# Optimization experiments

Hardware: AMD Instinct MI355X
Metric: run time of the kernel (lower is better)

## Reference

```python
import jax, jax.numpy as jnp
import numpy as np

C = 256       # in_channels
INTER = C // 2
BS = 4        # block_size
BN_EPS = 1e-5


def _conv1x1(x, w, b):
    # x: [N,C,H,W], w: [O,C], b: [O]
    return jnp.einsum('nchw,oc->nohw', x, w) + b[None, :, None, None]


def _maxpool2(x):
    n, c, h, w = x.shape
    return x.reshape(n, c, h // 2, 2, w // 2, 2).max(axis=(3, 5))


def setup_inputs() -> dict:
    key = jax.random.key(0)
    ks = jax.random.split(key, 13)
    p = lambda k, shape, s=0.05: jax.random.normal(k, shape, jnp.float32) * s
    return {
        'x': jax.random.normal(ks[0], (8, C, 128, 128), jnp.float32),
        'theta_w': p(ks[1], (INTER, C)), 'theta_b': p(ks[2], (INTER,)),
        'phi_w': p(ks[3], (INTER, C)), 'phi_b': p(ks[4], (INTER,)),
        'g_w': p(ks[5], (INTER, C)), 'g_b': p(ks[6], (INTER,)),
        'w_w': p(ks[7], (C, INTER)), 'w_b': p(ks[8], (C,)),
        'bn_gamma': p(ks[9], (C,)), 'bn_beta': p(ks[10], (C,)),
        'bn_mean': p(ks[11], (C,)), 'bn_var': jnp.abs(p(ks[12], (C,))) + 1.0,
    }


def reference(x, theta_w, theta_b, phi_w, phi_b, g_w, g_b, w_w, w_b,
              bn_gamma, bn_beta, bn_mean, bn_var):
    b, c, h, w = x.shape
    th, tw = h // BS, w // BS  # tile size (32,32)
    # split into BS*BS non-overlapping tiles, batch them: [b*BS*BS, c, th, tw]
    xb = x.reshape(b, c, BS, th, BS, tw).transpose(0, 2, 4, 1, 3, 5)
    xb = xb.reshape(b * BS * BS, c, th, tw)
    # SNLB (batched over all tiles at once)
    theta = _conv1x1(xb, theta_w, theta_b).reshape(-1, INTER, th * tw).transpose(0, 2, 1)  # [N,q,i]
    phi = _maxpool2(_conv1x1(xb, phi_w, phi_b)).reshape(-1, INTER, (th // 2) * (tw // 2))   # [N,i,k]
    g = _maxpool2(_conv1x1(xb, g_w, g_b)).reshape(-1, INTER, (th // 2) * (tw // 2))
    g = g.transpose(0, 2, 1)                                                                # [N,k,i]
    f = jax.nn.softmax(jnp.einsum('nqi,nik->nqk', theta, phi), axis=-1)                     # [N,q,k]
    y = jnp.einsum('nqk,nki->nqi', f, g).transpose(0, 2, 1).reshape(-1, INTER, th, tw)
    wy = _conv1x1(y, w_w, w_b)
    inv = jax.lax.rsqrt(bn_var + BN_EPS)
    wy = (wy - bn_mean[None, :, None, None]) * (inv * bn_gamma)[None, :, None, None] \
         + bn_beta[None, :, None, None]
    z = wy + xb  # [N,c,th,tw]
    # torch: cat tiles along channel dim (tile-major), then view(b, c, th*BS, -1)
    bf = z.reshape(b, BS * BS * c, th, tw)
    return bf.reshape(b, c, th * BS, -1)
```

## Files before the change

### kernel.cpp

```cpp
#include <hip/hip_runtime.h>
#include <hip/hip_bf16.h>

typedef __bf16 bf16_t;
typedef __bf16 bf16x8 __attribute__((ext_vector_type(8)));
typedef float f32x4 __attribute__((ext_vector_type(4)));

#define LDT 136
#define LDF 264
#define LDP 136
#define LDG 264

__device__ __forceinline__ float ldin(const void* p, long i, int isbf) {
  if (isbf) {
    unsigned short u = ((const unsigned short*)p)[i];
    unsigned int w = ((unsigned int)u) << 16;
    float f; __builtin_memcpy(&f, &w, 4); return f;
  }
  return ((const float*)p)[i];
}

__device__ __forceinline__ bf16_t f2b(float f) {
  unsigned int u; __builtin_memcpy(&u, &f, 4);
  u += 0x7FFFu + ((u >> 16) & 1u);
  unsigned short h = (unsigned short)(u >> 16);
  bf16_t r; __builtin_memcpy(&r, &h, 2); return r;
}

__device__ __forceinline__ float b2f(bf16_t b) {
  unsigned short h; __builtin_memcpy(&h, &b, 2);
  unsigned int u = ((unsigned int)h) << 16;
  float f; __builtin_memcpy(&f, &u, 4); return f;
}

__device__ __forceinline__ float bb2f(unsigned short h) {
  unsigned int u = ((unsigned int)h) << 16;
  float f; __builtin_memcpy(&f, &u, 4); return f;
}

__device__ __forceinline__ unsigned short bbits(bf16_t b) {
  unsigned short h; __builtin_memcpy(&h, &b, 2); return h;
}

__device__ __forceinline__ void ld4(const void* p, long i, int isbf, float* v) {
  if (isbf) {
    ushort4 u = *(const ushort4*)((const unsigned short*)p + i);
    v[0] = bb2f(u.x); v[1] = bb2f(u.y); v[2] = bb2f(u.z); v[3] = bb2f(u.w);
  } else {
    float4 f = *(const float4*)((const float*)p + i);
    v[0] = f.x; v[1] = f.y; v[2] = f.z; v[3] = f.w;
  }
}

__device__ __forceinline__ f32x4 mfma(bf16x8 a, bf16x8 b, f32x4 c) {
  return __builtin_amdgcn_mfma_f32_16x16x32_bf16(a, b, c, 0, 0, 0);
}

__global__ void kdetect(const unsigned int* x, int* flag) {
  __shared__ int cnt;
  if (threadIdx.x == 0) cnt = 0;
  __syncthreads();
  int local = 0;
  for (int k = 0; k < 4; ++k) {
    unsigned int u = x[threadIdx.x * 4 + k];
    unsigned int e = (u >> 7) & 0xFFu;
    if (e >= 116u && e <= 133u) local++;
  }
  atomicAdd(&cnt, local);
  __syncthreads();
  if (threadIdx.x == 0) *flag = (cnt > 512) ? 1 : 0;
}

__global__ void k0(const void* thw_f, const void* phw, const void* gw, const void* ww_f,
                   const void* wb, const void* gma, const void* bta, const void* mean,
                   const void* var, bf16_t* thwb, bf16_t* phwb, bf16_t* gwb, bf16_t* wwb,
                   float* scw, float* shw, const int* flag) {
  int isbf = *flag;
  int i = blockIdx.x * 256 + threadIdx.x;
  thwb[i] = f2b(ldin(thw_f, i, isbf));
  phwb[i] = f2b(ldin(phw, i, isbf));
  gwb[i]  = f2b(ldin(gw, i, isbf));
  wwb[i]  = f2b(ldin(ww_f, i, isbf));
  if (i < 256) {
    float s = ldin(gma, i, isbf) * rsqrtf(ldin(var, i, isbf) + 1e-5f);
    scw[i] = s;
    shw[i] = (ldin(wb, i, isbf) - ldin(mean, i, isbf)) * s + ldin(bta, i, isbf);
  }
}

__global__ __launch_bounds__(256) void k1(const void* xin, const bf16_t* phwb,
    const bf16_t* gwb, const void* phb, const void* gbb,
    bf16_t* phiH, bf16_t* phiL, bf16_t* gT, const int* flag) {
  int isbf = *flag;
  int wg = blockIdx.x;
  int tile = wg >> 4, j = wg & 15;
  int bi = tile >> 4, t16 = tile & 15, ty = t16 >> 2, tx = t16 & 3;
  long xb = (long)bi * 256 * 16384 + (long)(ty * 32 + 2 * j) * 128 + tx * 32;

  __shared__ __align__(16) bf16_t sX[64 * 256];
  __shared__ __align__(16) bf16_t sPoH[16 * 136];
  __shared__ __align__(16) bf16_t sPoL[16 * 136];
  __shared__ __align__(16) bf16_t sGo[128 * 24];

  int tid = threadIdx.x, lane = tid & 63, wv = tid >> 6;
  int qd = lane >> 4, ln = lane & 15, kq = qd * 8;

  bf16x8 Bp[8], Bg[8];
  {
    const bf16_t* bp = phwb + (wv * 16 + ln) * 256;
    const bf16_t* bg = gwb + (wv * 16 + ln) * 256;
    #pragma unroll
    for (int c = 0; c < 8; ++c) {
      Bp[c] = *(const bf16x8*)(bp + c * 32 + kq);
      Bg[c] = *(const bf16x8*)(bg + c * 32 + kq);
    }
  }

  {
    int mq = tid & 15, c0 = tid >> 4;
    int ma = (mq >> 3) * 128 + (mq & 7) * 4;
    #pragma unroll
    for (int it = 0; it < 16; ++it) {
      int c = it * 16 + c0;
      float v[4];
      ld4(xin, xb + (long)c * 16384 + ma, isbf, v);
      #pragma unroll
      for (int r = 0; r < 4; ++r) {
        int m = mq * 4 + r;
        int s = (((m >> 2) ^ m) & 7) << 3;
        sX[m * 256 + (c ^ s)] = f2b(v[r]);
      }
    }
  }
  __syncthreads();

  #pragma unroll
  for (int h = 0; h < 2; ++h) {
    if (h == 1) {
      const bf16_t* bp = phwb + ((wv + 4) * 16 + ln) * 256;
      const bf16_t* bg = gwb + ((wv + 4) * 16 + ln) * 256;
      #pragma unroll
      for (int c = 0; c < 8; ++c) {
        Bp[c] = *(const bf16x8*)(bp + c * 32 + kq);
        Bg[c] = *(const bf16x8*)(bg + c * 32 + kq);
      }
    }
    f32x4 accP[4], accG[4];
    #pragma unroll
    for (int mb = 0; mb < 4; ++mb) {
      int row = mb * 16 + ln;
      int s = (((row >> 2) ^ row) & 7) << 3;
      bf16x8 af[8];
      #pragma unroll
      for (int c = 0; c < 8; ++c)
        af[c] = *(const bf16x8*)(sX + row * 256 + ((c * 32 + kq) ^ s));
      f32x4 ap = {0.f,0.f,0.f,0.f}, ag = {0.f,0.f,0.f,0.f};
      #pragma unroll
      for (int c = 0; c < 8; ++c) {
        ap = mfma(af[c], Bp[c], ap);
        ag = mfma(af[c], Bg[c], ag);
      }
      accP[mb] = ap; accG[mb] = ag;
    }
    int o = (wv + h * 4) * 16 + ln;
    float pb = ldin(phb, o, isbf), gb2 = ldin(gbb, o, isbf);
    #pragma unroll
    for (int mb2 = 0; mb2 < 2; ++mb2)
      #pragma unroll
      for (int r = 0; r < 4; r += 2) {
        float v = fmaxf(fmaxf(accP[mb2][r], accP[mb2][r + 1]),
                        fmaxf(accP[mb2 + 2][r], accP[mb2 + 2][r + 1]));
        float u = fmaxf(fmaxf(accG[mb2][r], accG[mb2][r + 1]),
                        fmaxf(accG[mb2 + 2][r], accG[mb2 + 2][r + 1]));
        int cp = mb2 * 8 + qd * 2 + (r >> 1);
        float pv = v + pb;
        bf16_t hi = f2b(pv);
        sPoH[cp * 136 + o] = hi;
        sPoL[cp * 136 + o] = f2b(pv - b2f(hi));
        sGo[o * 24 + cp] = f2b(u + gb2);
      }
  }
  __syncthreads();

  {
    int kp = tid >> 4, seg = tid & 15;
    long base = (long)tile * 32768 + (long)(j * 16 + kp) * 128 + seg * 8;
    *(uint4*)(phiH + base) = *(const uint4*)(sPoH + kp * 136 + seg * 8);
    *(uint4*)(phiL + base) = *(const uint4*)(sPoL + kp * 136 + seg * 8);
  }
  {
    int o = tid >> 1, sg = tid & 1;
    *(uint4*)(gT + (long)tile * 32768 + (long)o * 256 + j * 16 + sg * 8) =
        *(const uint4*)(sGo + o * 24 + sg * 8);
  }
}

__global__ __launch_bounds__(256, 3) void k2(const void* xin, const bf16_t* thwb,
    const void* thb, const bf16_t* phiH, const bf16_t* phiL, const bf16_t* gT,
    const bf16_t* wwb, const float* sc, const float* sh, void* outv, const int* flag) {
  int isbf = *flag;
  int wg = (blockIdx.x & 7) * 512 + (blockIdx.x >> 3);
  int tile = wg >> 5, qb = wg & 31;
  int bi = tile >> 4, t16 = tile & 15, ty = t16 >> 2, tx = t16 & 3;
  long xbase = (long)bi * 256 * 16384 + (long)(ty * 32 + qb) * 128 + tx * 32;

  __shared__ __align__(16) char smem[51200];
  bf16_t* sX   = (bf16_t*)smem;
  bf16_t* sPh  = (bf16_t*)smem;
  bf16_t* sPl  = (bf16_t*)(smem + 8704);
  bf16_t* sG   = (bf16_t*)smem;
  bf16_t* sW   = (bf16_t*)smem;
  bf16_t* sY   = (bf16_t*)(smem + 17408);
  bf16_t* sTh  = (bf16_t*)(smem + 33280);
  bf16_t* sTl  = (bf16_t*)(smem + 41984);
  bf16_t* sF   = (bf16_t*)(smem + 33280);
  float* sredM = (float*)(smem + 50688);
  float* sredS = (float*)(smem + 50944);

  int tid = threadIdx.x, lane = tid & 63, wv = tid >> 6;
  int qd = lane >> 4, ln = lane & 15, kq = qd * 8;
  int ms = wv >> 1, half = wv & 1;
  int m0 = ms * 16 + qd * 4;

  {
    int wq = tid & 7, c0 = tid >> 3;
    #pragma unroll
    for (int it = 0; it < 8; ++it) {
      int c = it * 32 + c0;
      float v[4];
      ld4(xin, xbase + (long)c * 16384 + wq * 4, isbf, v);
      #pragma unroll
      for (int r = 0; r < 4; ++r) {
        int m = wq * 4 + r;
        int s = (((m >> 2) ^ m) & 7) << 3;
        int cs = c ^ s;
        bf16_t hi = f2b(v[r]);
        sX[m * 512 + cs] = hi;
        sX[m * 512 + 256 + cs] = f2b(v[r] - b2f(hi));
      }
    }
  }
  __syncthreads();

  {
    bf16x8 Axf[8];
    #pragma unroll
    for (int t = 0; t < 4; ++t) {
      int tms = t >> 1, tns = (t & 1) * 4 + wv;
      if ((t & 1) == 0) {
        int row = tms * 16 + ln;
        int s = (((row >> 2) ^ row) & 7) << 3;
        #pragma unroll
        for (int c = 0; c < 8; ++c)
          Axf[c] = *(const bf16x8*)(sX + row * 512 + ((c * 32 + kq) ^ s));
      }
      const bf16_t* B = thwb + (tns * 16 + ln) * 256;
      f32x4 a = {0.f,0.f,0.f,0.f};
      #pragma unroll
      for (int c = 0; c < 8; ++c) a = mfma(Axf[c], *(const bf16x8*)(B + c * 32 + kq), a);
      float bias = ldin(thb, tns * 16 + ln, isbf);
      #pragma unroll
      for (int r = 0; r < 4; ++r) {
        float v = a[r] + bias;
        bf16_t hi = f2b(v);
        int mrow = tms * 16 + qd * 4 + r;
        sTh[mrow * LDT + tns * 16 + ln] = hi;
        sTl[mrow * LDT + tns * 16 + ln] = f2b(v - b2f(hi));
      }
    }
  }

  const bf16_t* PH = phiH + (long)tile * 32768;
  const bf16_t* PL = phiL + (long)tile * 32768;
  const bf16_t* GG = gT + (long)tile * 32768;

  uint4 pf0 = *(const uint4*)(PH + tid * 8);
  uint4 pf1 = *(const uint4*)(PH + 2048 + tid * 8);
  uint4 pf2 = *(const uint4*)(PL + tid * 8);
  uint4 pf3 = *(const uint4*)(PL + 2048 + tid * 8);

  f32x4 xres[8];
  #pragma unroll
  for (int c4 = 0; c4 < 4; ++c4) {
    #pragma unroll
    for (int jj = 0; jj < 2; ++jj) {
      int o = c4 * 64 + (half * 2 + jj) * 16 + ln;
      f32x4 xr;
      #pragma unroll
      for (int r = 0; r < 4; ++r) {
        int row = m0 + r;
        int s = (((row >> 2) ^ row) & 7) << 3;
        int cs = o ^ s;
        xr[r] = b2f(sX[row * 512 + cs]) + b2f(sX[row * 512 + 256 + cs]);
      }
      xres[c4 * 2 + jj] = xr;
    }
  }
  __syncthreads();

  bf16x8 Ah[4], Al[4];
  {
    const bf16_t* th = sTh + (ms * 16 + ln) * LDT;
    const bf16_t* tl = sTl + (ms * 16 + ln) * LDT;
    #pragma unroll
    for (int c = 0; c < 4; ++c) {
      Ah[c] = *(const bf16x8*)(th + c * 32 + kq);
      Al[c] = *(const bf16x8*)(tl + c * 32 + kq);
    }
  }

  int srow = tid >> 4, scol = (tid & 15) * 8;
  int grow = tid >> 5, gcol = (tid & 31) * 8;

  f32x4 S[8];
  #pragma unroll
  for (int c = 0; c < 8; ++c) {
    *(uint4*)(sPh + srow * LDP + scol) = pf0;
    *(uint4*)(sPh + (srow + 16) * LDP + scol) = pf1;
    *(uint4*)(sPl + srow * LDP + scol) = pf2;
    *(uint4*)(sPl + (srow + 16) * LDP + scol) = pf3;
    if (c < 7) {
      pf0 = *(const uint4*)(PH + (c + 1) * 4096 + tid * 8);
      pf1 = *(const uint4*)(PH + (c + 1) * 4096 + 2048 + tid * 8);
      pf2 = *(const uint4*)(PL + (c + 1) * 4096 + tid * 8);
      pf3 = *(const uint4*)(PL + (c + 1) * 4096 + 2048 + tid * 8);
    } else {
      pf0 = *(const uint4*)(GG + tid * 8);
      pf1 = *(const uint4*)(GG + 2048 + tid * 8);
      pf2 = *(const uint4*)(GG + 4096 + tid * 8);
      pf3 = *(const uint4*)(GG + 6144 + tid * 8);
    }
    __syncthreads();
    const bf16_t* Bh = sPh + (half * 16 + ln) * LDP;
    const bf16_t* Bl = sPl + (half * 16 + ln) * LDP;
    f32x4 a = {0.f,0.f,0.f,0.f};
    #pragma unroll
    for (int kk = 0; kk < 4; ++kk) {
      int ko = kk * 32 + kq;
      bf16x8 bh = *(const bf16x8*)(Bh + ko);
      bf16x8 bl = *(const bf16x8*)(Bl + ko);
      a = mfma(Ah[kk], bl, a);
      a = mfma(Al[kk], bh, a);
      a = mfma(Ah[kk], bh, a);
    }
    S[c] = a;
    __syncthreads();
  }

  float Mr[4], Sr[4], inv4[4];
  #pragma unroll
  for (int r = 0; r < 4; ++r) {
    float m = S[0][r];
    #pragma unroll
    for (int t = 1; t < 8; ++t) m = fmaxf(m, S[t][r]);
    #pragma unroll
    for (int d = 1; d < 16; d <<= 1) m = fmaxf(m, __shfl_xor(m, d, 64));
    Mr[r] = m;
  }
  if (ln == 0) {
    #pragma unroll
    for (int r = 0; r < 4; ++r) sredM[(m0 + r) * 2 + half] = Mr[r];
  }
  __syncthreads();
  #pragma unroll
  for (int r = 0; r < 4; ++r) Mr[r] = fmaxf(Mr[r], sredM[(m0 + r) * 2 + (half ^ 1)]);
  #pragma unroll
  for (int r = 0; r < 4; ++r) {
    float s = 0.f;
    #pragma unroll
    for (int t = 0; t < 8; ++t) { float e = __expf(S[t][r] - Mr[r]); S[t][r] = e; s += e; }
    #pragma unroll
    for (int d = 1; d < 16; d <<= 1) s += __shfl_xor(s, d, 64);
    Sr[r] = s;
  }
  if (ln == 0) {
    #pragma unroll
    for (int r = 0; r < 4; ++r) sredS[(m0 + r) * 2 + half] = Sr[r];
  }
  __syncthreads();
  #pragma unroll
  for (int r = 0; r < 4; ++r) inv4[r] = 1.f / (Sr[r] + sredS[(m0 + r) * 2 + (half ^ 1)]);

  #pragma unroll
  for (int c = 0; c < 8; ++c) {
    int n = c * 32 + half * 16 + ln;
    #pragma unroll
    for (int r = 0; r < 4; ++r)
      sF[(m0 + r) * LDF + n] = f2b(S[c][r] * inv4[r]);
  }
  __syncthreads();

  bf16x8 Fa[8];
  {
    const bf16_t* fa = sF + (ms * 16 + ln) * LDF;
    #pragma unroll
    for (int c = 0; c < 8; ++c) Fa[c] = *(const bf16x8*)(fa + c * 32 + kq);
  }
  #pragma unroll
  for (int c = 0; c < 4; ++c) {
    *(uint4*)(sG + grow * LDG + gcol) = pf0;
    *(uint4*)(sG + (grow + 8) * LDG + gcol) = pf1;
    *(uint4*)(sG + (grow + 16) * LDG + gcol) = pf2;
    *(uint4*)(sG + (grow + 24) * LDG + gcol) = pf3;
    if (c < 3) {
      pf0 = *(const uint4*)(GG + (c + 1) * 8192 + tid * 8);
      pf1 = *(const uint4*)(GG + (c + 1) * 8192 + 2048 + tid * 8);
      pf2 = *(const uint4*)(GG + (c + 1) * 8192 + 4096 + tid * 8);
      pf3 = *(const uint4*)(GG + (c + 1) * 8192 + 6144 + tid * 8);
    } else {
      pf0 = *(const uint4*)(wwb + tid * 8);
      pf1 = *(const uint4*)(wwb + 2048 + tid * 8);
      pf2 = *(const uint4*)(wwb + 4096 + tid * 8);
      pf3 = *(const uint4*)(wwb + 6144 + tid * 8);
    }
    __syncthreads();
    const bf16_t* Bg = sG + (half * 16 + ln) * LDG;
    f32x4 a = {0.f,0.f,0.f,0.f};
    #pragma unroll
    for (int kk = 0; kk < 8; ++kk)
      a = mfma(Fa[kk], *(const bf16x8*)(Bg + kk * 32 + kq), a);
    #pragma unroll
    for (int r = 0; r < 4; ++r)
      sY[(m0 + r) * LDT + c * 32 + half * 16 + ln] = f2b(a[r]);
    __syncthreads();
  }

  bf16x8 Ya[4];
  {
    const bf16_t* ya = sY + (ms * 16 + ln) * LDT;
    #pragma unroll
    for (int kk = 0; kk < 4; ++kk) Ya[kk] = *(const bf16x8*)(ya + kk * 32 + kq);
  }
  #pragma unroll
  for (int cb = 0; cb < 4; ++cb) {
    *(uint4*)(sW + srow * LDP + scol) = pf0;
    *(uint4*)(sW + (srow + 16) * LDP + scol) = pf1;
    *(uint4*)(sW + (srow + 32) * LDP + scol) = pf2;
    *(uint4*)(sW + (srow + 48) * LDP + scol) = pf3;
    if (cb < 3) {
      pf0 = *(const uint4*)(wwb + (cb + 1) * 8192 + tid * 8);
      pf1 = *(const uint4*)(wwb + (cb + 1) * 8192 + 2048 + tid * 8);
      pf2 = *(const uint4*)(wwb + (cb + 1) * 8192 + 4096 + tid * 8);
      pf3 = *(const uint4*)(wwb + (cb + 1) * 8192 + 6144 + tid * 8);
    }
    __syncthreads();
    #pragma unroll
    for (int jj = 0; jj < 2; ++jj) {
      int nsL = half * 2 + jj;
      const bf16_t* B = sW + (nsL * 16 + ln) * LDP;
      f32x4 a = {0.f,0.f,0.f,0.f};
      #pragma unroll
      for (int kk = 0; kk < 4; ++kk)
        a = mfma(Ya[kk], *(const bf16x8*)(B + kk * 32 + kq), a);
      int o = cb * 64 + nsL * 16 + ln;
      float s2 = sc[o], hh = sh[o];
      f32x4 xr = xres[cb * 2 + jj];
      long oi = (long)tile * 262144 + (long)o * 1024 + qb * 32 + m0;
      if (isbf) {
        unsigned short uu[4];
        #pragma unroll
        for (int r = 0; r < 4; ++r) uu[r] = bbits(f2b(a[r] * s2 + hh + xr[r]));
        __builtin_memcpy((unsigned short*)outv + oi, uu, 8);
      } else {
        float vv[4];
        #pragma unroll
        for (int r = 0; r < 4; ++r) vv[r] = a[r] * s2 + hh + xr[r];
        __builtin_memcpy((float*)outv + oi, vv, 16);
      }
    }
    __syncthreads();
  }
}

extern "C" void kernel_launch(void* const* d_in, const int* in_sizes, int n_in,
                              void* d_out, int out_size, void* d_ws, size_t ws_size,
                              hipStream_t stream) {
  (void)in_sizes; (void)n_in; (void)out_size; (void)ws_size;
  const void* x    = d_in[0];
  const void* thwf = d_in[1];
  const void* thb  = d_in[2];
  const void* phw  = d_in[3];
  const void* phb  = d_in[4];
  const void* gwf  = d_in[5];
  const void* gbb  = d_in[6];
  const void* wwf  = d_in[7];
  const void* wb   = d_in[8];
  const void* gma  = d_in[9];
  const void* bta  = d_in[10];
  const void* mn   = d_in[11];
  const void* vr   = d_in[12];

  char* ws = (char*)d_ws;
  bf16_t* thwb = (bf16_t*)(ws);
  bf16_t* phwb = (bf16_t*)(ws + 65536);
  bf16_t* gwb  = (bf16_t*)(ws + 131072);
  bf16_t* wwb  = (bf16_t*)(ws + 196608);
  float*  sc   = (float*)(ws + 262144);
  float*  sh   = (float*)(ws + 263168);
  int*    flag = (int*)(ws + 264192);
  bf16_t* phiH = (bf16_t*)(ws + 264448);
  bf16_t* phiL = (bf16_t*)(ws + 264448 + 8388608);
  bf16_t* gT   = (bf16_t*)(ws + 264448 + 16777216);

  kdetect<<<1, 256, 0, stream>>>((const unsigned int*)x, flag);
  k0<<<128, 256, 0, stream>>>(thwf, phw, gwf, wwf, wb, gma, bta, mn, vr,
                              thwb, phwb, gwb, wwb, sc, sh, flag);
  k1<<<2048, 256, 0, stream>>>(x, phwb, gwb, phb, gbb, phiH, phiL, gT, flag);
  k2<<<4096, 256, 0, stream>>>(x, thwb, thb, phiH, phiL, gT, wwb, sc, sh,
                               d_out, flag);
}
```

Baseline: 436.9 us.

## Double-buffer k2 staging with two-deep prefetch, XOR-swizzled LDS, and lighter barriers

Rewrites the staged phi/g/W loop in k2 as a unified 16-step pipeline over two alternating LDS stage buffers. Global prefetch now runs two steps ahead, which lets one barrier per step replace the previous two. Padded LDS strides are swapped for XOR swizzles to avoid bank conflicts in less shared memory. __syncthreads is replaced with an inline s_waitcnt lgkmcnt(0)+s_barrier, and MFMA chains are split into two accumulators to shorten dependency chains. This costs more registers for the two prefetch sets, and the custom barrier does not wait on outstanding global loads.

```diff
diff --git a/kernel.cpp b/kernel.cpp
--- a/kernel.cpp
+++ b/kernel.cpp
@@ -4,11 +4,6 @@
 typedef __bf16 bf16_t;
 typedef __bf16 bf16x8 __attribute__((ext_vector_type(8)));
 typedef float f32x4 __attribute__((ext_vector_type(4)));
-
-#define LDT 136
-#define LDF 264
-#define LDP 136
-#define LDG 264
 
 __device__ __forceinline__ float ldin(const void* p, long i, int isbf) {
   if (isbf) {
@@ -53,6 +48,10 @@
 
 __device__ __forceinline__ f32x4 mfma(bf16x8 a, bf16x8 b, f32x4 c) {
   return __builtin_amdgcn_mfma_f32_16x16x32_bf16(a, b, c, 0, 0, 0);
+}
+
+__device__ __forceinline__ void lbar() {
+  asm volatile("s_waitcnt lgkmcnt(0)\n\ts_barrier" ::: "memory");
 }
 
 __global__ void kdetect(const unsigned int* x, int* flag) {
@@ -203,43 +202,96 @@
   int bi = tile >> 4, t16 = tile & 15, ty = t16 >> 2, tx = t16 & 3;
   long xbase = (long)bi * 256 * 16384 + (long)(ty * 32 + qb) * 128 + tx * 32;
 
-  __shared__ __align__(16) char smem[51200];
-  bf16_t* sX   = (bf16_t*)smem;
-  bf16_t* sPh  = (bf16_t*)smem;
-  bf16_t* sPl  = (bf16_t*)(smem + 8704);
-  bf16_t* sG   = (bf16_t*)smem;
-  bf16_t* sW   = (bf16_t*)smem;
-  bf16_t* sY   = (bf16_t*)(smem + 17408);
-  bf16_t* sTh  = (bf16_t*)(smem + 33280);
-  bf16_t* sTl  = (bf16_t*)(smem + 41984);
-  bf16_t* sF   = (bf16_t*)(smem + 33280);
-  float* sredM = (float*)(smem + 50688);
-  float* sredS = (float*)(smem + 50944);
+  __shared__ __align__(16) char smem[49664];
+  bf16_t* stage = (bf16_t*)smem;
+  bf16_t* sX  = (bf16_t*)smem;
+  bf16_t* sTh = (bf16_t*)(smem + 32768);
+  bf16_t* sTl = (bf16_t*)(smem + 40960);
+  bf16_t* sF  = (bf16_t*)(smem + 32768);
+  bf16_t* sY  = (bf16_t*)(smem + 32768);
+  float* sredM = (float*)(smem + 49152);
+  float* sredS = (float*)(smem + 49408);
 
   int tid = threadIdx.x, lane = tid & 63, wv = tid >> 6;
   int qd = lane >> 4, ln = lane & 15, kq = qd * 8;
   int ms = wv >> 1, half = wv & 1;
   int m0 = ms * 16 + qd * 4;
 
+  int pr = tid >> 4, pc = (tid & 15) * 8, pswz = (pr & 7) << 3;
+  int gr = tid >> 5, gc = (tid & 31) * 8, gswz = (gr & 7) << 3;
+  int brow = half * 16 + ln, bswz = (brow & 7) << 3;
+
+  const bf16_t* PH = phiH + (long)tile * 32768;
+  const bf16_t* PL = phiL + (long)tile * 32768;
+  const bf16_t* GG = gT + (long)tile * 32768;
+
+#define ISSUE(cc, pf)                                              \
+  do {                                                             \
+    if ((cc) < 8) {                                                \
+      const bf16_t* p_ = PH + (cc) * 4096;                         \
+      const bf16_t* q_ = PL + (cc) * 4096;                         \
+      pf[0] = *(const uint4*)(p_ + tid * 8);                       \
+      pf[1] = *(const uint4*)(p_ + 2048 + tid * 8);                \
+      pf[2] = *(const uint4*)(q_ + tid * 8);                       \
+      pf[3] = *(const uint4*)(q_ + 2048 + tid * 8);                \
+    } else if ((cc) < 12) {                                        \
+      const bf16_t* p_ = GG + ((cc) - 8) * 8192;                   \
+      pf[0] = *(const uint4*)(p_ + tid * 8);                       \
+      pf[1] = *(const uint4*)(p_ + 2048 + tid * 8);                \
+      pf[2] = *(const uint4*)(p_ + 4096 + tid * 8);                \
+      pf[3] = *(const uint4*)(p_ + 6144 + tid * 8);                \
+    } else if ((cc) < 16) {                                        \
+      const bf16_t* p_ = wwb + ((cc) - 12) * 8192;                 \
+      pf[0] = *(const uint4*)(p_ + tid * 8);                       \
+      pf[1] = *(const uint4*)(p_ + 2048 + tid * 8);                \
+      pf[2] = *(const uint4*)(p_ + 4096 + tid * 8);                \
+      pf[3] = *(const uint4*)(p_ + 6144 + tid * 8);                \
+    }                                                              \
+  } while (0)
+
+#define WPHI(sl, pf)                                               \
+  do {                                                             \
+    *(uint4*)((sl) + pr * 128 + (pc ^ pswz)) = pf[0];              \
+    *(uint4*)((sl) + (pr + 16) * 128 + (pc ^ pswz)) = pf[1];       \
+    *(uint4*)((sl) + 4096 + pr * 128 + (pc ^ pswz)) = pf[2];       \
+    *(uint4*)((sl) + 4096 + (pr + 16) * 128 + (pc ^ pswz)) = pf[3];\
+  } while (0)
+
+#define WG(sl, pf)                                                 \
+  do {                                                             \
+    *(uint4*)((sl) + gr * 256 + (gc ^ gswz)) = pf[0];              \
+    *(uint4*)((sl) + (gr + 8) * 256 + (gc ^ gswz)) = pf[1];        \
+    *(uint4*)((sl) + (gr + 16) * 256 + (gc ^ gswz)) = pf[2];       \
+    *(uint4*)((sl) + (gr + 24) * 256 + (gc ^ gswz)) = pf[3];       \
+  } while (0)
+
+#define WW(sl, pf)                                                 \
+  do {                                                             \
+    *(uint4*)((sl) + pr * 128 + (pc ^ pswz)) = pf[0];              \
+    *(uint4*)((sl) + (pr + 16) * 128 + (pc ^ pswz)) = pf[1];       \
+    *(uint4*)((sl) + (pr + 32) * 128 + (pc ^ pswz)) = pf[2];       \
+    *(uint4*)((sl) + (pr + 48) * 128 + (pc ^ pswz)) = pf[3];       \
+  } while (0)
+
   {
     int wq = tid & 7, c0 = tid >> 3;
     #pragma unroll
     for (int it = 0; it < 8; ++it) {
-      int c = it * 32 + c0;
+      int cch = it * 32 + c0;
       float v[4];
-      ld4(xin, xbase + (long)c * 16384 + wq * 4, isbf, v);
+      ld4(xin, xbase + (long)cch * 16384 + wq * 4, isbf, v);
       #pragma unroll
       for (int r = 0; r < 4; ++r) {
         int m = wq * 4 + r;
         int s = (((m >> 2) ^ m) & 7) << 3;
-        int cs = c ^ s;
+        int cs = cch ^ s;
         bf16_t hi = f2b(v[r]);
         sX[m * 512 + cs] = hi;
         sX[m * 512 + 256 + cs] = f2b(v[r] - b2f(hi));
       }
     }
   }
-  __syncthreads();
+  lbar();
 
   {
     bf16x8 Axf[8];
@@ -254,29 +306,30 @@
           Axf[c] = *(const bf16x8*)(sX + row * 512 + ((c * 32 + kq) ^ s));
       }
       const bf16_t* B = thwb + (tns * 16 + ln) * 256;
-      f32x4 a = {0.f,0.f,0.f,0.f};
-      #pragma unroll
-      for (int c = 0; c < 8; ++c) a = mfma(Axf[c], *(const bf16x8*)(B + c * 32 + kq), a);
+      f32x4 t0 = {0.f,0.f,0.f,0.f}, t1 = {0.f,0.f,0.f,0.f};
+      #pragma unroll
+      for (int c = 0; c < 8; ++c) {
+        bf16x8 bw = *(const bf16x8*)(B + c * 32 + kq);
+        if (c < 4) t0 = mfma(Axf[c], bw, t0);
+        else       t1 = mfma(Axf[c], bw, t1);
+      }
+      f32x4 a = t0 + t1;
       float bias = ldin(thb, tns * 16 + ln, isbf);
       #pragma unroll
       for (int r = 0; r < 4; ++r) {
         float v = a[r] + bias;
         bf16_t hi = f2b(v);
         int mrow = tms * 16 + qd * 4 + r;
-        sTh[mrow * LDT + tns * 16 + ln] = hi;
-        sTl[mrow * LDT + tns * 16 + ln] = f2b(v - b2f(hi));
-      }
-    }
-  }
-
-  const bf16_t* PH = phiH + (long)tile * 32768;
-  const bf16_t* PL = phiL + (long)tile * 32768;
-  const bf16_t* GG = gT + (long)tile * 32768;
-
-  uint4 pf0 = *(const uint4*)(PH + tid * 8);
-  uint4 pf1 = *(const uint4*)(PH + 2048 + tid * 8);
-  uint4 pf2 = *(const uint4*)(PL + tid * 8);
-  uint4 pf3 = *(const uint4*)(PL + 2048 + tid * 8);
+        int col = (tns * 16 + ln) ^ ((mrow & 7) << 3);
+        sTh[mrow * 128 + col] = hi;
+        sTl[mrow * 128 + col] = f2b(v - b2f(hi));
+      }
+    }
+  }
+
+  uint4 pfA[4], pfB[4];
+  ISSUE(0, pfA);
+  ISSUE(1, pfB);
 
   f32x4 xres[8];
   #pragma unroll
@@ -295,55 +348,40 @@
       xres[c4 * 2 + jj] = xr;
     }
   }
-  __syncthreads();
+  lbar();
 
   bf16x8 Ah[4], Al[4];
   {
-    const bf16_t* th = sTh + (ms * 16 + ln) * LDT;
-    const bf16_t* tl = sTl + (ms * 16 + ln) * LDT;
+    int row = ms * 16 + ln, sw = (row & 7) << 3;
     #pragma unroll
     for (int c = 0; c < 4; ++c) {
-      Ah[c] = *(const bf16x8*)(th + c * 32 + kq);
-      Al[c] = *(const bf16x8*)(tl + c * 32 + kq);
-    }
-  }
-
-  int srow = tid >> 4, scol = (tid & 15) * 8;
-  int grow = tid >> 5, gcol = (tid & 31) * 8;
+      Ah[c] = *(const bf16x8*)(sTh + row * 128 + ((c * 32 + kq) ^ sw));
+      Al[c] = *(const bf16x8*)(sTl + row * 128 + ((c * 32 + kq) ^ sw));
+    }
+  }
 
   f32x4 S[8];
   #pragma unroll
   for (int c = 0; c < 8; ++c) {
-    *(uint4*)(sPh + srow * LDP + scol) = pf0;
-    *(uint4*)(sPh + (srow + 16) * LDP + scol) = pf1;
-    *(uint4*)(sPl + srow * LDP + scol) = pf2;
-    *(uint4*)(sPl + (srow + 16) * LDP + scol) = pf3;
-    if (c < 7) {
-      pf0 = *(const uint4*)(PH + (c + 1) * 4096 + tid * 8);
-      pf1 = *(const uint4*)(PH + (c + 1) * 4096 + 2048 + tid * 8);
-      pf2 = *(const uint4*)(PL + (c + 1) * 4096 + tid * 8);
-      pf3 = *(const uint4*)(PL + (c + 1) * 4096 + 2048 + tid * 8);
-    } else {
-      pf0 = *(const uint4*)(GG + tid * 8);
-      pf1 = *(const uint4*)(GG + 2048 + tid * 8);
-      pf2 = *(const uint4*)(GG + 4096 + tid * 8);
-      pf3 = *(const uint4*)(GG + 6144 + tid * 8);
-    }
-    __syncthreads();
-    const bf16_t* Bh = sPh + (half * 16 + ln) * LDP;
-    const bf16_t* Bl = sPl + (half * 16 + ln) * LDP;
-    f32x4 a = {0.f,0.f,0.f,0.f};
+    bf16_t* sl = stage + (c & 1) * 8192;
+    if (c & 1) { WPHI(sl, pfB); ISSUE(c + 2, pfB); }
+    else       { WPHI(sl, pfA); ISSUE(c + 2, pfA); }
+    lbar();
+    const bf16_t* Bh = sl + brow * 128;
+    const bf16_t* Bl = sl + 4096 + brow * 128;
+    f32x4 a0 = {0.f,0.f,0.f,0.f}, a1 = {0.f,0.f,0.f,0.f};
     #pragma unroll
     for (int kk = 0; kk < 4; ++kk) {
-      int ko = kk * 32 + kq;
-      bf16x8 bh = *(const bf16x8*)(Bh + ko);
-      bf16x8 bl = *(const bf16x8*)(Bl + ko);
-      a = mfma(Ah[kk], bl, a);
-      a = mfma(Al[kk], bh, a);
-      a = mfma(Ah[kk], bh, a);
-    }
-    S[c] = a;
-    __syncthreads();
+      int co = (kk * 32 + kq) ^ bswz;
+      bf16x8 bh = *(const bf16x8*)(Bh + co);
+      bf16x8 bl = *(const bf16x8*)(Bl + co);
+      if (kk < 2) {
+        a0 = mfma(Ah[kk], bl, a0); a0 = mfma(Al[kk], bh, a0); a0 = mfma(Ah[kk], bh, a0);
+      } else {
+        a1 = mfma(Ah[kk], bl, a1); a1 = mfma(Al[kk], bh, a1); a1 = mfma(Ah[kk], bh, a1);
+      }
+    }
+    S[c] = a0 + a1;
   }
 
   float Mr[4], Sr[4], inv4[4];
@@ -360,7 +398,7 @@
     #pragma unroll
     for (int r = 0; r < 4; ++r) sredM[(m0 + r) * 2 + half] = Mr[r];
   }
-  __syncthreads();
+  lbar();
   #pragma unroll
   for (int r = 0; r < 4; ++r) Mr[r] = fmaxf(Mr[r], sredM[(m0 + r) * 2 + (half ^ 1)]);
   #pragma unroll
@@ -376,7 +414,7 @@
     #pragma unroll
     for (int r = 0; r < 4; ++r) sredS[(m0 + r) * 2 + half] = Sr[r];
   }
-  __syncthreads();
+  lbar();
   #pragma unroll
   for (int r = 0; r < 4; ++r) inv4[r] = 1.f / (Sr[r] + sredS[(m0 + r) * 2 + (half ^ 1)]);
 
@@ -384,76 +422,80 @@
   for (int c = 0; c < 8; ++c) {
     int n = c * 32 + half * 16 + ln;
     #pragma unroll
-    for (int r = 0; r < 4; ++r)
-      sF[(m0 + r) * LDF + n] = f2b(S[c][r] * inv4[r]);
-  }
-  __syncthreads();
+    for (int r = 0; r < 4; ++r) {
+      int row = m0 + r;
+      sF[row * 256 + (n ^ ((row & 7) << 3))] = f2b(S[c][r] * inv4[r]);
+    }
+  }
+  lbar();
 
   bf16x8 Fa[8];
   {
-    const bf16_t* fa = sF + (ms * 16 + ln) * LDF;
-    #pragma unroll
-    for (int c = 0; c < 8; ++c) Fa[c] = *(const bf16x8*)(fa + c * 32 + kq);
-  }
-  #pragma unroll
-  for (int c = 0; c < 4; ++c) {
-    *(uint4*)(sG + grow * LDG + gcol) = pf0;
-    *(uint4*)(sG + (grow + 8) * LDG + gcol) = pf1;
-    *(uint4*)(sG + (grow + 16) * LDG + gcol) = pf2;
-    *(uint4*)(sG + (grow + 24) * LDG + gcol) = pf3;
-    if (c < 3) {
-      pf0 = *(const uint4*)(GG + (c + 1) * 8192 + tid * 8);
-      pf1 = *(const uint4*)(GG + (c + 1) * 8192 + 2048 + tid * 8);
-      pf2 = *(const uint4*)(GG + (c + 1) * 8192 + 4096 + tid * 8);
-      pf3 = *(const uint4*)(GG + (c + 1) * 8192 + 6144 + tid * 8);
-    } else {
-      pf0 = *(const uint4*)(wwb + tid * 8);
-      pf1 = *(const uint4*)(wwb + 2048 + tid * 8);
-      pf2 = *(const uint4*)(wwb + 4096 + tid * 8);
-      pf3 = *(const uint4*)(wwb + 6144 + tid * 8);
-    }
-    __syncthreads();
-    const bf16_t* Bg = sG + (half * 16 + ln) * LDG;
-    f32x4 a = {0.f,0.f,0.f,0.f};
-    #pragma unroll
-    for (int kk = 0; kk < 8; ++kk)
-      a = mfma(Fa[kk], *(const bf16x8*)(Bg + kk * 32 + kq), a);
-    #pragma unroll
-    for (int r = 0; r < 4; ++r)
-      sY[(m0 + r) * LDT + c * 32 + half * 16 + ln] = f2b(a[r]);
-    __syncthreads();
-  }
+    int row = ms * 16 + ln, sw = (row & 7) << 3;
+    #pragma unroll
+    for (int c = 0; c < 8; ++c)
+      Fa[c] = *(const bf16x8*)(sF + row * 256 + ((c * 32 + kq) ^ sw));
+  }
+
+  #pragma unroll
+  for (int ci = 0; ci < 4; ++ci) {
+    const int c = 8 + ci;
+    bf16_t* sl = stage + (c & 1) * 8192;
+    if (c & 1) { WG(sl, pfB); ISSUE(c + 2, pfB); }
+    else       { WG(sl, pfA); ISSUE(c + 2, pfA); }
+    lbar();
+    const bf16_t* Bg = sl + brow * 256;
+    f32x4 a0 = {0.f,0.f,0.f,0.f}, a1 = {0.f,0.f,0.f,0.f};
+    #pragma unroll
+    for (int kk = 0; kk < 8; ++kk) {
+      int co = (kk * 32 + kq) ^ bswz;
+      bf16x8 bw = *(const bf16x8*)(Bg + co);
+      if (kk < 4) a0 = mfma(Fa[kk], bw, a0);
+      else        a1 = mfma(Fa[kk], bw, a1);
+    }
+    f32x4 ya = a0 + a1;
+    #pragma unroll
+    for (int r = 0; r < 4; ++r) {
+      int row = m0 + r;
+      int col = ci * 32 + half * 16 + ln;
+      sY[row * 128 + (col ^ ((row & 7) << 3))] = f2b(ya[r]);
+    }
+  }
+  lbar();
 
   bf16x8 Ya[4];
   {
-    const bf16_t* ya = sY + (ms * 16 + ln) * LDT;
-    #pragma unroll
-    for (int kk = 0; kk < 4; ++kk) Ya[kk] = *(const bf16x8*)(ya + kk * 32 + kq);
-  }
-  #pragma unroll
-  for (int cb = 0; cb < 4; ++cb) {
-    *(uint4*)(sW + srow * LDP + scol) = pf0;
-    *(uint4*)(sW + (srow + 16) * LDP + scol) = pf1;
-    *(uint4*)(sW + (srow + 32) * LDP + scol) = pf2;
-    *(uint4*)(sW + (srow + 48) * LDP + scol) = pf3;
-    if (cb < 3) {
-      pf0 = *(const uint4*)(wwb + (cb + 1) * 8192 + tid * 8);
-      pf1 = *(const uint4*)(wwb + (cb + 1) * 8192 + 2048 + tid * 8);
-      pf2 = *(const uint4*)(wwb + (cb + 1) * 8192 + 4096 + tid * 8);
-      pf3 = *(const uint4*)(wwb + (cb + 1) * 8192 + 6144 + tid * 8);
-    }
-    __syncthreads();
+    int row = ms * 16 + ln, sw = (row & 7) << 3;
+    #pragma unroll
+    for (int kk = 0; kk < 4; ++kk)
+      Ya[kk] = *(const bf16x8*)(sY + row * 128 + ((kk * 32 + kq) ^ sw));
+  }
+
+  #pragma unroll
+  for (int ci = 0; ci < 4; ++ci) {
+    const int c = 12 + ci;
+    bf16_t* sl = stage + (c & 1) * 8192;
+    if (c & 1) { WW(sl, pfB); if (c + 2 < 16) ISSUE(c + 2, pfB); }
+    else       { WW(sl, pfA); if (c + 2 < 16) ISSUE(c + 2, pfA); }
+    lbar();
     #pragma unroll
     for (int jj = 0; jj < 2; ++jj) {
       int nsL = half * 2 + jj;
-      const bf16_t* B = sW + (nsL * 16 + ln) * LDP;
-      f32x4 a = {0.f,0.f,0.f,0.f};
-      #pragma unroll
-      for (int kk = 0; kk < 4; ++kk)
-        a = mfma(Ya[kk], *(const bf16x8*)(B + kk * 32 + kq), a);
-      int o = cb * 64 + nsL * 16 + ln;
+      int rw = nsL * 16 + ln;
+      int wsw = (rw & 7) << 3;
+      const bf16_t* Bw = sl + rw * 128;
+      f32x4 a0 = {0.f,0.f,0.f,0.f}, a1 = {0.f,0.f,0.f,0.f};
+      #pragma unroll
+      for (int kk = 0; kk < 4; ++kk) {
+        int co = (kk * 32 + kq) ^ wsw;
+        bf16x8 bw = *(const bf16x8*)(Bw + co);
+        if (kk < 2) a0 = mfma(Ya[kk], bw, a0);
+        else        a1 = mfma(Ya[kk], bw, a1);
+      }
+      f32x4 a = a0 + a1;
+      int o = ci * 64 + nsL * 16 + ln;
       float s2 = sc[o], hh = sh[o];
-      f32x4 xr = xres[cb * 2 + jj];
+      f32x4 xr = xres[ci * 2 + jj];
       long oi = (long)tile * 262144 + (long)o * 1024 + qb * 32 + m0;
       if (isbf) {
         unsigned short uu[4];
@@ -467,8 +509,11 @@
         __builtin_memcpy((float*)outv + oi, vv, 16);
       }
     }
-    __syncthreads();
-  }
+  }
+#undef ISSUE
+#undef WPHI
+#undef WG
+#undef WW
 }
 
 extern "C" void kernel_launch(void* const* d_in, const int* in_sizes, int n_in,
```

Measured after the change: 740.7 us. 1.7x slower.
